# Kernel optimization log

Hardware: AMD Instinct MI355X
Metric: run time of the kernel (lower is better)

## Reference

```python
import jax, jax.numpy as jnp
import numpy as np

ALPHA = 0.7
EPS = 1e-12


def setup_inputs() -> dict:
    key = jax.random.key(0)
    k1, k2, k3, k4 = jax.random.split(key, 4)
    B, P, D = 4, 256, 384  # dinov2_vits14: 224/14=16 -> 256 patches, dim 384
    N, M = 100000, 2000    # local memory bank (max_memory), global bank (train images)
    return {
        "patches": jax.random.normal(k1, (B, P, D), dtype=jnp.float32),
        "globals_x": jax.random.normal(k2, (B, D), dtype=jnp.float32),
        "mb_local": jax.random.normal(k3, (N, D), dtype=jnp.float32),
        "mb_global": jax.random.normal(k4, (M, D), dtype=jnp.float32),
    }


def _l2_normalize(x):
    return x / (jnp.linalg.norm(x, axis=-1, keepdims=True) + EPS)


def reference(patches, globals_x, mb_local, mb_global):
    # Token normalization as in _extract_patch_tokens / _extract_global
    p = _l2_normalize(patches)    # [B, P, D]
    g = _l2_normalize(globals_x)  # [B, D]

    # Local: Euclidean cdist(p_i, MB_local) via gram trick, min over bank, max over patches
    p_sq = jnp.sum(p * p, axis=-1)                      # [B, P]
    mbl_sq = jnp.sum(mb_local * mb_local, axis=-1)      # [N]
    d2 = (p_sq[..., None] + mbl_sq[None, None, :]
          - 2.0 * jnp.einsum('bpd,nd->bpn', p, mb_local))  # [B, P, N]
    d = jnp.sqrt(jnp.maximum(d2, 0.0))
    local_score = jnp.max(jnp.min(d, axis=2), axis=1)   # [B]

    # Global: cdist(g_i, MB_global).min()
    g_sq = jnp.sum(g * g, axis=-1)                      # [B]
    mbg_sq = jnp.sum(mb_global * mb_global, axis=-1)    # [M]
    gd2 = g_sq[:, None] + mbg_sq[None, :] - 2.0 * (g @ mb_global.T)  # [B, M]
    gdist = jnp.min(jnp.sqrt(jnp.maximum(gd2, 0.0)), axis=1)         # [B]

    return ALPHA * local_score + (1.0 - ALPHA) * gdist  # [B] anomaly scores
```

## Files before the change

kernel.cpp:

```cpp
#include <hip/hip_runtime.h>
#include <math.h>


#define D 384
#define PQ 256
#define TNP 128
#define BK 64
#define LROW 72

typedef __attribute__((ext_vector_type(8))) short short8v;
typedef __attribute__((ext_vector_type(4))) float f32x4;

static __device__ __forceinline__ unsigned short f2bf(float f) {
  unsigned u = __float_as_uint(f);
  unsigned r = 0x7FFFu + ((u >> 16) & 1u);
  return (unsigned short)((u + r) >> 16);
}
static __device__ __forceinline__ unsigned pack2(float lo, float hi) {
  return (unsigned)f2bf(lo) | ((unsigned)f2bf(hi) << 16);
}

__global__ void prep_kernel(const float* __restrict__ patches,
                            const float* __restrict__ globals_x,
                            float* __restrict__ pf32,
                            unsigned short* __restrict__ pbf,
                            float* __restrict__ psq,
                            float* __restrict__ gf32,
                            float* __restrict__ gsq,
                            int Q) {
  const int row = blockIdx.x;
  const int lane = threadIdx.x;
  const float* src = (row < Q) ? (patches + (size_t)row * D)
                               : (globals_x + (size_t)(row - Q) * D);
  float v[6];
  float ss = 0.f;
#pragma unroll
  for (int j = 0; j < 6; ++j) { v[j] = src[lane + 64 * j]; ss += v[j] * v[j]; }
#pragma unroll
  for (int d = 1; d < 64; d <<= 1) ss += __shfl_xor(ss, d);
  const float inv = 1.f / (sqrtf(ss) + 1e-12f);
  float pn[6]; float ps = 0.f;
#pragma unroll
  for (int j = 0; j < 6; ++j) { pn[j] = v[j] * inv; ps += pn[j] * pn[j]; }
#pragma unroll
  for (int d = 1; d < 64; d <<= 1) ps += __shfl_xor(ps, d);
  if (row < Q) {
#pragma unroll
    for (int j = 0; j < 6; ++j) {
      pf32[(size_t)row * D + lane + 64 * j] = pn[j];
      pbf[(size_t)row * D + lane + 64 * j] = f2bf(pn[j]);
    }
    if (lane == 0) psq[row] = ps;
  } else {
    const int b = row - Q;
#pragma unroll
    for (int j = 0; j < 6; ++j) gf32[(size_t)b * D + lane + 64 * j] = pn[j];
    if (lane == 0) gsq[b] = ps;
  }
}

__device__ __forceinline__ void atomic_fmin(float* addr, float val) {
  unsigned* ua = (unsigned*)addr;
  float cur = __uint_as_float(atomicAdd(ua, 0u));
  while (val < cur) {
    unsigned assumed = __float_as_uint(cur);
    unsigned old = atomicCAS(ua, assumed, __float_as_uint(val));
    if (old == assumed) break;
    cur = __uint_as_float(old);
  }
}

template <int MODE>
__global__ __launch_bounds__(256, 2) void score_kernel(
    const float* __restrict__ mbl,
    const unsigned short* __restrict__ pbf,
    float* __restrict__ tilemin,
    int Q, int N, int NSUBP, int QP, int q8, int r8) {
  __shared__ alignas(16) unsigned short lB0[TNP * LROW];
  __shared__ alignas(16) unsigned short lB1[TNP * LROW];
  __shared__ float msqH[TNP * 2];
  __shared__ float msqF[TNP];

  const int tid = threadIdx.x;
  const int lane = tid & 63;
  const int wid = tid >> 6;
  const int fr = lane & 15;
  const int g = lane >> 4;

  const int flat = blockIdx.x;
  const int xcd = flat & 7, idx = flat >> 3;
  const int wg = (xcd < r8 ? xcd * (q8 + 1) : r8 * (q8 + 1) + (xcd - r8) * q8) + idx;
  const int nb = wg / QP;
  const int qp = wg - nb * QP;
  const int qbase = qp * PQ;
  const int nbase = nb * TNP;

  const int brow = tid >> 1, h = tid & 1;
  const int gn = nbase + brow;
  const float* bptr = mbl + (size_t)((gn < N) ? gn : 0) * D + h * 32;
  const int boff = brow * LROW + h * 32;

  const unsigned short* abase = pbf + (size_t)(qbase + wid * 64 + fr) * D + g * 8;

  f32x4 acc[4][8];
#pragma unroll
  for (int i = 0; i < 4; ++i)
#pragma unroll
    for (int j = 0; j < 8; ++j) acc[i][j] = (f32x4){0.f, 0.f, 0.f, 0.f};
  float msqreg = 0.f;
  float4 breg[8];
  short8v a[8];

  auto bload = [&](int kc) {
    const float* src = bptr + kc * BK;
#pragma unroll
    for (int i = 0; i < 8; ++i) breg[i] = *(const float4*)(src + i * 4);
  };
  auto bwrite = [&](unsigned short* base) {
    float s = 0.f;
    uint4 w[4];
#pragma unroll
    for (int i = 0; i < 4; ++i) {
      float4 f0 = breg[2 * i], f1 = breg[2 * i + 1];
      s += f0.x*f0.x + f0.y*f0.y + f0.z*f0.z + f0.w*f0.w
         + f1.x*f1.x + f1.y*f1.y + f1.z*f1.z + f1.w*f1.w;
      w[i] = (uint4){ pack2(f0.x,f0.y), pack2(f0.z,f0.w), pack2(f1.x,f1.y), pack2(f1.z,f1.w) };
    }
#pragma unroll
    for (int i = 0; i < 4; ++i) *(uint4*)(base + boff + i * 8) = w[i];
    msqreg += s;
  };
  auto aload = [&](int kc) {
#pragma unroll
    for (int ks = 0; ks < 2; ++ks)
#pragma unroll
      for (int mf = 0; mf < 4; ++mf)
        a[ks * 4 + mf] = *(const short8v*)(abase + (size_t)mf * 16 * D + kc * BK + ks * 32);
  };
  auto compute = [&](const unsigned short* buf) {
#pragma unroll
    for (int ks = 0; ks < 2; ++ks) {
#pragma unroll
      for (int half = 0; half < 2; ++half) {
        short8v b4[4];
#pragma unroll
        for (int nf = 0; nf < 4; ++nf)
          b4[nf] = *(const short8v*)(&buf[((half * 4 + nf) * 16 + fr) * LROW + (ks * 4 + g) * 8]);
#pragma unroll
        for (int mf = 0; mf < 4; ++mf)
#pragma unroll
          for (int nf = 0; nf < 4; ++nf)
            acc[mf][half * 4 + nf] = __builtin_amdgcn_mfma_f32_16x16x32_bf16(
                a[ks * 4 + mf], b4[nf], acc[mf][half * 4 + nf], 0, 0, 0);
      }
    }
  };

  bload(0);
  bwrite(lB0);
  __syncthreads();
  aload(0); bload(1); compute(lB0); bwrite(lB1); __syncthreads();
  aload(1); bload(2); compute(lB1); bwrite(lB0); __syncthreads();
  aload(2); bload(3); compute(lB0); bwrite(lB1); __syncthreads();
  aload(3); bload(4); compute(lB1); bwrite(lB0); __syncthreads();
  aload(4); bload(5); compute(lB0); bwrite(lB1); __syncthreads();
  aload(5);           compute(lB1);              __syncthreads();

  msqH[tid] = msqreg;
  __syncthreads();
  if (tid < TNP) msqF[tid] = (nbase + tid < N) ? (msqH[2 * tid] + msqH[2 * tid + 1]) : 1e30f;
  __syncthreads();

  float mq[8];
#pragma unroll
  for (int nf = 0; nf < 8; ++nf) mq[nf] = msqF[nf * 16 + fr];

#pragma unroll
  for (int mf = 0; mf < 4; ++mf) {
#pragma unroll
    for (int j = 0; j < 4; ++j) {
      float v[4];
#pragma unroll
      for (int s = 0; s < 4; ++s)
        v[s] = fminf(mq[2 * s] - 2.f * acc[mf][2 * s][j],
                     mq[2 * s + 1] - 2.f * acc[mf][2 * s + 1][j]);
#pragma unroll
      for (int d2 = 1; d2 < 16; d2 <<= 1)
#pragma unroll
        for (int s = 0; s < 4; ++s) v[s] = fminf(v[s], __shfl_xor(v[s], d2));
      if (fr == 0) {
        const int q = qbase + wid * 64 + mf * 16 + g * 4 + j;
        if (MODE == 0) {
          *(float4*)&tilemin[(size_t)q * NSUBP + nb * 4] =
              (float4){v[0], v[1], v[2], v[3]};
        } else {
          atomic_fmin(&tilemin[q],
                      fminf(fminf(v[0], v[1]), fminf(v[2], v[3])));
        }
      }
    }
  }
}

__global__ void init_inf_kernel(float* __restrict__ p, int n) {
  int i = blockIdx.x * 256 + threadIdx.x;
  if (i < n) p[i] = 1e30f;
}
__global__ void final_dmin_kernel(const float* __restrict__ d2min,
                                  const float* __restrict__ psq,
                                  float* __restrict__ dmin, int Q) {
  int q = blockIdx.x * 256 + threadIdx.x;
  if (q < Q) dmin[q] = sqrtf(fmaxf(psq[q] + d2min[q], 0.f));
}

__device__ __forceinline__ float block_min(float v, float* red) {
#pragma unroll
  for (int d = 1; d < 64; d <<= 1) v = fminf(v, __shfl_xor(v, d));
  if ((threadIdx.x & 63) == 0) red[threadIdx.x >> 6] = v;
  __syncthreads();
  const float r = fminf(fminf(red[0], red[1]), fminf(red[2], red[3]));
  __syncthreads();
  return r;
}
__device__ __forceinline__ float block_max(float v, float* red) {
#pragma unroll
  for (int d = 1; d < 64; d <<= 1) v = fmaxf(v, __shfl_xor(v, d));
  if ((threadIdx.x & 63) == 0) red[threadIdx.x >> 6] = v;
  __syncthreads();
  const float r = fmaxf(fmaxf(red[0], red[1]), fmaxf(red[2], red[3]));
  __syncthreads();
  return r;
}

__global__ __launch_bounds__(256) void refine_kernel(
    const float* __restrict__ mbl,
    const float* __restrict__ pf32,
    const float* __restrict__ psq,
    const float* __restrict__ tm,
    float* __restrict__ dmin,
    int Q, int N, int NSUB, int NSUBP) {
  __shared__ int cnt;
  __shared__ int cand[64];
  __shared__ float red[4];
  const int q = blockIdx.x;
  const int tid = threadIdx.x;
  if (tid == 0) cnt = 0;
  __syncthreads();

  const float* rowp = tm + (size_t)q * NSUBP;
  float m = 1e30f;
  for (int r = tid; r < NSUB; r += 256) m = fminf(m, rowp[r]);
  const float gm = block_min(m, red);
  const float thr = gm + 0.25f;

  for (int r = tid; r < NSUB; r += 256)
    if (rowp[r] <= thr) { int i = atomicAdd(&cnt, 1); if (i < 64) cand[i] = r; }
  __syncthreads();
  const int nc = min(cnt, 64);

  const int row8 = tid >> 3, oct = tid & 7;
  const float* prow = pf32 + (size_t)q * D + oct * 48;
  float4 pr[12];
#pragma unroll
  for (int i = 0; i < 12; ++i) pr[i] = *(const float4*)(prow + i * 4);

  float best = 1e30f;
  for (int c = 0; c < nc; ++c) {
    const int n = cand[c] * 32 + row8;
    float v;
    if (n < N) {
      const float* mr = mbl + (size_t)n * D + oct * 48;
      float dot = 0.f, ms = 0.f;
#pragma unroll
      for (int i = 0; i < 12; ++i) {
        float4 aa = *(const float4*)(mr + i * 4);
        dot += aa.x*pr[i].x + aa.y*pr[i].y + aa.z*pr[i].z + aa.w*pr[i].w;
        ms  += aa.x*aa.x + aa.y*aa.y + aa.z*aa.z + aa.w*aa.w;
      }
      v = ms - 2.f * dot;
    } else {
      v = 1e30f;
    }
#pragma unroll
    for (int d2 = 1; d2 < 8; d2 <<= 1) {
      float o = __shfl_xor(v, d2);
      v = (n < N) ? v + o : 1e30f;
    }
    best = fminf(best, v);
  }
  best = block_min(best, red);
  if (tid == 0) dmin[q] = sqrtf(fmaxf(psq[q] + best, 0.f));
}

__global__ __launch_bounds__(256) void gmin_kernel(
    const float* __restrict__ mbg,
    const float* __restrict__ gf32,
    const float* __restrict__ gsq,
    float* __restrict__ gpartG,
    int M) {
  __shared__ float red[4];
  const int b = blockIdx.x, s = blockIdx.y;
  const int tid = threadIdx.x;
  const int sl = (M + 31) / 32;
  const int row = s * sl + tid;
  const float* g = gf32 + (size_t)b * D;
  float v = 1e30f;
  if (tid < sl && row < M) {
    const float* mr = mbg + (size_t)row * D;
    float dot = 0.f, ms = 0.f;
#pragma unroll 4
    for (int k = 0; k < D; k += 4) {
      float4 aa = *(const float4*)(mr + k);
      float4 p = *(const float4*)(g + k);
      dot += aa.x*p.x + aa.y*p.y + aa.z*p.z + aa.w*p.w;
      ms  += aa.x*aa.x + aa.y*aa.y + aa.z*aa.z + aa.w*aa.w;
    }
    v = gsq[b] + ms - 2.f * dot;
  }
  v = block_min(v, red);
  if (tid == 0) gpartG[b * 32 + s] = v;
}

__global__ __launch_bounds__(256) void out_kernel(
    const float* __restrict__ gpartG,
    const float* __restrict__ dmin,
    float* __restrict__ out,
    int P) {
  __shared__ float red[4];
  const int b = blockIdx.x;
  const int tid = threadIdx.x;
  float v = (tid < P) ? dmin[(size_t)b * P + tid] : -1e30f;
  const float local = block_max(v, red);
  float gm = (tid < 32) ? gpartG[b * 32 + tid] : 1e30f;
  gm = block_min(gm, red);
  if (tid == 0) out[b] = 0.7f * local + 0.3f * sqrtf(fmaxf(gm, 0.f));
}

extern "C" void kernel_launch(void* const* d_in, const int* in_sizes, int n_in,
                              void* d_out, int out_size, void* d_ws, size_t ws_size,
                              hipStream_t stream) {
  const float* patches   = (const float*)d_in[0];
  const float* globals_x = (const float*)d_in[1];
  const float* mbl       = (const float*)d_in[2];
  const float* mbg       = (const float*)d_in[3];
  float* out = (float*)d_out;

  const int Q = in_sizes[0] / D;
  const int B = in_sizes[1] / D;
  const int N = in_sizes[2] / D;
  const int M = in_sizes[3] / D;
  const int P = Q / B;
  const int NPAN = (N + TNP - 1) / TNP;
  const int NSUB = NPAN * 4;
  const int NSUBP = ((NSUB + 63) / 64) * 64;
  const int QP = (Q + PQ - 1) / PQ;
  const int nwg = QP * NPAN;
  const int q8 = nwg / 8, r8 = nwg % 8;

  char* w = (char*)d_ws;
  char* wend = (char*)d_ws + ws_size;
  auto alloc = [&](size_t bytes) {
    char* p = w;
    w += (bytes + 255) & ~(size_t)255;
    return p;
  };
  float*          pf32   = (float*)alloc((size_t)Q * D * sizeof(float));
  unsigned short* pbf    = (unsigned short*)alloc((size_t)Q * D * sizeof(unsigned short));
  float*          psq    = (float*)alloc((size_t)Q * sizeof(float));
  float*          gf32   = (float*)alloc((size_t)B * D * sizeof(float));
  float*          gsqp   = (float*)alloc((size_t)B * sizeof(float));
  float*          dmin   = (float*)alloc((size_t)Q * sizeof(float));
  float*          gpartG = (float*)alloc((size_t)B * 32 * sizeof(float));
  float*          d2min  = (float*)alloc((size_t)Q * sizeof(float));
  if (w > wend) return;

  const size_t tm_bytes = (size_t)Q * NSUBP * sizeof(float);
  const int full = (w + ((tm_bytes + 255) & ~(size_t)255) <= wend) ? 1 : 0;

  prep_kernel<<<Q + B, 64, 0, stream>>>(patches, globals_x, pf32, pbf, psq, gf32, gsqp, Q);

  if (full) {
    float* tilemin = (float*)alloc(tm_bytes);
    score_kernel<0><<<nwg, 256, 0, stream>>>(mbl, pbf, tilemin, Q, N, NSUBP, QP, q8, r8);
    refine_kernel<<<Q, 256, 0, stream>>>(mbl, pf32, psq, tilemin, dmin, Q, N, NSUB, NSUBP);
  } else {
    init_inf_kernel<<<(Q + 255) / 256, 256, 0, stream>>>(d2min, Q);
    score_kernel<1><<<nwg, 256, 0, stream>>>(mbl, pbf, d2min, Q, N, NSUBP, QP, q8, r8);
    final_dmin_kernel<<<(Q + 255) / 256, 256, 0, stream>>>(d2min, psq, dmin, Q);
  }

  gmin_kernel<<<dim3(B, 32), 256, 0, stream>>>(mbg, gf32, gsqp, gpartG, M);
  out_kernel<<<B, 256, 0, stream>>>(gpartG, dmin, out, P);
}
```

Measured before the change: 457.4 us.

## Pre-convert memory bank to bf16 once and split refine over segments

Adds a convert kernel that turns the fp32 local memory bank into padded bf16 rows plus precomputed squared norms. The score kernel, which reloads each bank panel for every query panel, now streams half the bytes and skips conversion and norm math. The refine kernel is split into four segments per query that combine through an atomic min, raising parallelism. The trade-offs are an extra pass over the bank, extra workspace, and a per-segment candidate threshold that may refine more candidates than before.

```diff
diff --git a/kernel.cpp b/kernel.cpp
--- a/kernel.cpp
+++ b/kernel.cpp
@@ -59,6 +59,42 @@
   }
 }
 
+__global__ __launch_bounds__(256) void convert_kernel(
+    const float* __restrict__ mbl,
+    unsigned short* __restrict__ bf16c,
+    float* __restrict__ msqg,
+    int N) {
+  const int nb = blockIdx.x;
+  const int tid = threadIdx.x;
+  const int r = tid >> 1, h = tid & 1;
+  const int gn = nb * TNP + r;
+  const bool ok = gn < N;
+  const float* src = mbl + (size_t)(ok ? gn : 0) * D + h * 32;
+  unsigned short* dst = bf16c + (size_t)gn * D + h * 32;
+  float s = 0.f;
+#pragma unroll
+  for (int kc = 0; kc < 6; ++kc) {
+    uint4 w[4];
+    if (ok) {
+#pragma unroll
+      for (int i = 0; i < 4; ++i) {
+        float4 f0 = *(const float4*)(src + kc * BK + i * 8);
+        float4 f1 = *(const float4*)(src + kc * BK + i * 8 + 4);
+        s += f0.x*f0.x + f0.y*f0.y + f0.z*f0.z + f0.w*f0.w
+           + f1.x*f1.x + f1.y*f1.y + f1.z*f1.z + f1.w*f1.w;
+        w[i] = (uint4){ pack2(f0.x,f0.y), pack2(f0.z,f0.w), pack2(f1.x,f1.y), pack2(f1.z,f1.w) };
+      }
+    } else {
+#pragma unroll
+      for (int i = 0; i < 4; ++i) w[i] = (uint4){0u,0u,0u,0u};
+    }
+#pragma unroll
+    for (int i = 0; i < 4; ++i) *(uint4*)(dst + kc * BK + i * 8) = w[i];
+  }
+  s += __shfl_xor(s, 1);
+  if (h == 0) msqg[gn] = ok ? s : 1e30f;
+}
+
 __device__ __forceinline__ void atomic_fmin(float* addr, float val) {
   unsigned* ua = (unsigned*)addr;
   float cur = __uint_as_float(atomicAdd(ua, 0u));
@@ -70,16 +106,14 @@
   }
 }
 
-template <int MODE>
 __global__ __launch_bounds__(256, 2) void score_kernel(
-    const float* __restrict__ mbl,
+    const unsigned short* __restrict__ bf16c,
     const unsigned short* __restrict__ pbf,
+    const float* __restrict__ msqg,
     float* __restrict__ tilemin,
-    int Q, int N, int NSUBP, int QP, int q8, int r8) {
+    int Q, int NSUBP, int QP, int q8, int r8) {
   __shared__ alignas(16) unsigned short lB0[TNP * LROW];
   __shared__ alignas(16) unsigned short lB1[TNP * LROW];
-  __shared__ float msqH[TNP * 2];
-  __shared__ float msqF[TNP];
 
   const int tid = threadIdx.x;
   const int lane = tid & 63;
@@ -96,10 +130,113 @@
   const int nbase = nb * TNP;
 
   const int brow = tid >> 1, h = tid & 1;
+  const unsigned short* bptr = bf16c + (size_t)(nbase + brow) * D + h * 32;
+  const int boff = brow * LROW + h * 32;
+
+  const unsigned short* abase = pbf + (size_t)(qbase + wid * 64 + fr) * D + g * 8;
+
+  f32x4 acc[4][8];
+#pragma unroll
+  for (int i = 0; i < 4; ++i)
+#pragma unroll
+    for (int j = 0; j < 8; ++j) acc[i][j] = (f32x4){0.f, 0.f, 0.f, 0.f};
+  uint4 st[4];
+  short8v a[8];
+
+  auto bload = [&](int kc) {
+#pragma unroll
+    for (int i = 0; i < 4; ++i) st[i] = *(const uint4*)(bptr + kc * BK + i * 8);
+  };
+  auto bwr = [&](unsigned short* base) {
+#pragma unroll
+    for (int i = 0; i < 4; ++i) *(uint4*)(base + boff + i * 8) = st[i];
+  };
+  auto aload = [&](int kc) {
+#pragma unroll
+    for (int ks = 0; ks < 2; ++ks)
+#pragma unroll
+      for (int mf = 0; mf < 4; ++mf)
+        a[ks * 4 + mf] = *(const short8v*)(abase + (size_t)mf * 16 * D + kc * BK + ks * 32);
+  };
+  auto compute = [&](const unsigned short* buf) {
+#pragma unroll
+    for (int ks = 0; ks < 2; ++ks) {
+#pragma unroll
+      for (int half = 0; half < 2; ++half) {
+        short8v b4[4];
+#pragma unroll
+        for (int nf = 0; nf < 4; ++nf)
+          b4[nf] = *(const short8v*)(&buf[((half * 4 + nf) * 16 + fr) * LROW + (ks * 4 + g) * 8]);
+#pragma unroll
+        for (int mf = 0; mf < 4; ++mf)
+#pragma unroll
+          for (int nf = 0; nf < 4; ++nf)
+            acc[mf][half * 4 + nf] = __builtin_amdgcn_mfma_f32_16x16x32_bf16(
+                a[ks * 4 + mf], b4[nf], acc[mf][half * 4 + nf], 0, 0, 0);
+      }
+    }
+  };
+
+  bload(0); bwr(lB0);
+  __syncthreads();
+  aload(0); bload(1); compute(lB0); bwr(lB1); __syncthreads();
+  aload(1); bload(2); compute(lB1); bwr(lB0); __syncthreads();
+  aload(2); bload(3); compute(lB0); bwr(lB1); __syncthreads();
+  aload(3); bload(4); compute(lB1); bwr(lB0); __syncthreads();
+  aload(4); bload(5); compute(lB0); bwr(lB1); __syncthreads();
+  aload(5);           compute(lB1);
+
+  float mq[8];
+#pragma unroll
+  for (int nf = 0; nf < 8; ++nf) mq[nf] = msqg[nbase + nf * 16 + fr];
+
+#pragma unroll
+  for (int mf = 0; mf < 4; ++mf) {
+#pragma unroll
+    for (int j = 0; j < 4; ++j) {
+      float v[4];
+#pragma unroll
+      for (int s = 0; s < 4; ++s)
+        v[s] = fminf(mq[2 * s] - 2.f * acc[mf][2 * s][j],
+                     mq[2 * s + 1] - 2.f * acc[mf][2 * s + 1][j]);
+#pragma unroll
+      for (int d2 = 1; d2 < 16; d2 <<= 1)
+#pragma unroll
+        for (int s = 0; s < 4; ++s) v[s] = fminf(v[s], __shfl_xor(v[s], d2));
+      if (fr == 0) {
+        const int q = qbase + wid * 64 + mf * 16 + g * 4 + j;
+        *(float4*)&tilemin[(size_t)q * NSUBP + nb * 4] = (float4){v[0], v[1], v[2], v[3]};
+      }
+    }
+  }
+}
+
+__global__ __launch_bounds__(256, 2) void score_fb_kernel(
+    const float* __restrict__ mbl,
+    const unsigned short* __restrict__ pbf,
+    float* __restrict__ d2min,
+    int Q, int N, int QP, int q8, int r8) {
+  __shared__ alignas(16) unsigned short lB0[TNP * LROW];
+  __shared__ alignas(16) unsigned short lB1[TNP * LROW];
+  __shared__ float msqH[TNP * 2];
+  __shared__ float msqF[TNP];
+
+  const int tid = threadIdx.x;
+  const int lane = tid & 63;
+  const int wid = tid >> 6;
+  const int fr = lane & 15;
+  const int g = lane >> 4;
+  const int flat = blockIdx.x;
+  const int xcd = flat & 7, idx = flat >> 3;
+  const int wg = (xcd < r8 ? xcd * (q8 + 1) : r8 * (q8 + 1) + (xcd - r8) * q8) + idx;
+  const int nb = wg / QP;
+  const int qp = wg - nb * QP;
+  const int qbase = qp * PQ;
+  const int nbase = nb * TNP;
+  const int brow = tid >> 1, h = tid & 1;
   const int gn = nbase + brow;
   const float* bptr = mbl + (size_t)((gn < N) ? gn : 0) * D + h * 32;
   const int boff = brow * LROW + h * 32;
-
   const unsigned short* abase = pbf + (size_t)(qbase + wid * 64 + fr) * D + g * 8;
 
   f32x4 acc[4][8];
@@ -139,7 +276,7 @@
   };
   auto compute = [&](const unsigned short* buf) {
 #pragma unroll
-    for (int ks = 0; ks < 2; ++ks) {
+    for (int ks = 0; ks < 2; ++ks)
 #pragma unroll
       for (int half = 0; half < 2; ++half) {
         short8v b4[4];
@@ -153,12 +290,9 @@
             acc[mf][half * 4 + nf] = __builtin_amdgcn_mfma_f32_16x16x32_bf16(
                 a[ks * 4 + mf], b4[nf], acc[mf][half * 4 + nf], 0, 0, 0);
       }
-    }
-  };
-
-  bload(0);
-  bwrite(lB0);
-  __syncthreads();
+  };
+
+  bload(0); bwrite(lB0); __syncthreads();
   aload(0); bload(1); compute(lB0); bwrite(lB1); __syncthreads();
   aload(1); bload(2); compute(lB1); bwrite(lB0); __syncthreads();
   aload(2); bload(3); compute(lB0); bwrite(lB1); __syncthreads();
@@ -190,13 +324,7 @@
         for (int s = 0; s < 4; ++s) v[s] = fminf(v[s], __shfl_xor(v[s], d2));
       if (fr == 0) {
         const int q = qbase + wid * 64 + mf * 16 + g * 4 + j;
-        if (MODE == 0) {
-          *(float4*)&tilemin[(size_t)q * NSUBP + nb * 4] =
-              (float4){v[0], v[1], v[2], v[3]};
-        } else {
-          atomic_fmin(&tilemin[q],
-                      fminf(fminf(v[0], v[1]), fminf(v[2], v[3])));
-        }
+        atomic_fmin(&d2min[q], fminf(fminf(v[0], v[1]), fminf(v[2], v[3])));
       }
     }
   }
@@ -235,25 +363,28 @@
 __global__ __launch_bounds__(256) void refine_kernel(
     const float* __restrict__ mbl,
     const float* __restrict__ pf32,
-    const float* __restrict__ psq,
     const float* __restrict__ tm,
-    float* __restrict__ dmin,
+    float* __restrict__ d2min,
     int Q, int N, int NSUB, int NSUBP) {
   __shared__ int cnt;
   __shared__ int cand[64];
   __shared__ float red[4];
   const int q = blockIdx.x;
+  const int seg = blockIdx.y;
   const int tid = threadIdx.x;
   if (tid == 0) cnt = 0;
   __syncthreads();
 
+  const int SEG = (NSUB + 3) >> 2;
+  const int r0 = seg * SEG;
+  const int r1 = min(NSUB, r0 + SEG);
   const float* rowp = tm + (size_t)q * NSUBP;
   float m = 1e30f;
-  for (int r = tid; r < NSUB; r += 256) m = fminf(m, rowp[r]);
+  for (int r = r0 + tid; r < r1; r += 256) m = fminf(m, rowp[r]);
   const float gm = block_min(m, red);
   const float thr = gm + 0.25f;
 
-  for (int r = tid; r < NSUB; r += 256)
+  for (int r = r0 + tid; r < r1; r += 256)
     if (rowp[r] <= thr) { int i = atomicAdd(&cnt, 1); if (i < 64) cand[i] = r; }
   __syncthreads();
   const int nc = min(cnt, 64);
@@ -289,7 +420,7 @@
     best = fminf(best, v);
   }
   best = block_min(best, red);
-  if (tid == 0) dmin[q] = sqrtf(fmaxf(psq[q] + best, 0.f));
+  if (tid == 0) atomic_fmin(&d2min[q], best);
 }
 
 __global__ __launch_bounds__(256) void gmin_kernel(
@@ -351,6 +482,7 @@
   const int M = in_sizes[3] / D;
   const int P = Q / B;
   const int NPAN = (N + TNP - 1) / TNP;
+  const int NPAD = NPAN * TNP;
   const int NSUB = NPAN * 4;
   const int NSUBP = ((NSUB + 63) / 64) * 64;
   const int QP = (Q + PQ - 1) / PQ;
@@ -374,21 +506,27 @@
   float*          d2min  = (float*)alloc((size_t)Q * sizeof(float));
   if (w > wend) return;
 
-  const size_t tm_bytes = (size_t)Q * NSUBP * sizeof(float);
-  const int full = (w + ((tm_bytes + 255) & ~(size_t)255) <= wend) ? 1 : 0;
-
+  const size_t bf16c_b = (size_t)NPAD * D * sizeof(unsigned short);
+  const size_t msqg_b  = (size_t)NPAD * sizeof(float);
+  const size_t tm_b    = (size_t)Q * NSUBP * sizeof(float);
+  const size_t need = ((bf16c_b + 255) & ~(size_t)255) + ((msqg_b + 255) & ~(size_t)255) +
+                      ((tm_b + 255) & ~(size_t)255);
+  const int full = ((size_t)(wend - w) >= need) ? 1 : 0;
+
+  init_inf_kernel<<<(Q + 255) / 256, 256, 0, stream>>>(d2min, Q);
   prep_kernel<<<Q + B, 64, 0, stream>>>(patches, globals_x, pf32, pbf, psq, gf32, gsqp, Q);
 
   if (full) {
-    float* tilemin = (float*)alloc(tm_bytes);
-    score_kernel<0><<<nwg, 256, 0, stream>>>(mbl, pbf, tilemin, Q, N, NSUBP, QP, q8, r8);
-    refine_kernel<<<Q, 256, 0, stream>>>(mbl, pf32, psq, tilemin, dmin, Q, N, NSUB, NSUBP);
+    unsigned short* bf16c = (unsigned short*)alloc(bf16c_b);
+    float*          msqg  = (float*)alloc(msqg_b);
+    float*          tm    = (float*)alloc(tm_b);
+    convert_kernel<<<NPAN, 256, 0, stream>>>(mbl, bf16c, msqg, N);
+    score_kernel<<<nwg, 256, 0, stream>>>(bf16c, pbf, msqg, tm, Q, NSUBP, QP, q8, r8);
+    refine_kernel<<<dim3(Q, 4), 256, 0, stream>>>(mbl, pf32, tm, d2min, Q, N, NSUB, NSUBP);
   } else {
-    init_inf_kernel<<<(Q + 255) / 256, 256, 0, stream>>>(d2min, Q);
-    score_kernel<1><<<nwg, 256, 0, stream>>>(mbl, pbf, d2min, Q, N, NSUBP, QP, q8, r8);
-    final_dmin_kernel<<<(Q + 255) / 256, 256, 0, stream>>>(d2min, psq, dmin, Q);
-  }
-
+    score_fb_kernel<<<nwg, 256, 0, stream>>>(mbl, pbf, d2min, Q, N, QP, q8, r8);
+  }
+  final_dmin_kernel<<<(Q + 255) / 256, 256, 0, stream>>>(d2min, psq, dmin, Q);
   gmin_kernel<<<dim3(B, 32), 256, 0, stream>>>(mbg, gf32, gsqp, gpartG, M);
   out_kernel<<<B, 256, 0, stream>>>(gpartG, dmin, out, P);
 }
```

Measured after the change: 477.1 us. +4.3%, slower.
